# Kernel optimization log

Hardware: AMD Instinct MI355X
Metric: run time of the kernel (lower is better)

## Reference

```python
import jax, jax.numpy as jnp
import numpy as np

TEMPERATURE = 0.1
NUM_CLASSES = 100


def setup_inputs() -> dict:
    key = jax.random.key(0)
    k1, k2 = jax.random.split(key)
    embeddings = jax.random.normal(k1, (8192, 128), dtype=jnp.float32)
    labels = jax.random.randint(k2, (8192,), 0, NUM_CLASSES, dtype=jnp.int64)
    return {"embeddings": embeddings, "labels": labels}


def reference(embeddings, labels):
    # L2-normalize rows (eps matches torch.nn.functional.normalize clamp)
    norm = jnp.maximum(jnp.linalg.norm(embeddings, axis=1, keepdims=True), 1e-12)
    e = embeddings / norm
    sim = jnp.matmul(e, e.T) / TEMPERATURE  # [N, N]
    n = sim.shape[0]
    eye = jnp.eye(n, dtype=bool)
    # positives: same label, excluding self
    pos = (labels[None, :] == labels[:, None]) & ~eye
    # The per-row torch loop computes soft-target cross-entropy over all
    # non-diagonal entries: row_loss_i = -sum_{j in pos(i)} log_softmax(sim[i, j!=i])_j.
    # log_softmax is permutation-invariant, so concatenation order is irrelevant.
    neg_inf = jnp.finfo(sim.dtype).min
    masked = jnp.where(eye, neg_inf, sim)
    logz = jax.nn.logsumexp(masked, axis=1, keepdims=True)  # [N, 1]
    logp = sim - logz  # [N, N]
    row_loss = -jnp.sum(jnp.where(pos, logp, 0.0), axis=1)  # rows with no positives contribute 0
    return jnp.sum(row_loss) / n
```

## Files before the change

kernel.cpp:

```cpp
#include <hip/hip_runtime.h>


#define N 8192
#define D 128
#define NCLS 100
#define RLCAP 256
#define JSPLIT 32
#define IBLK 256
#define NJT ((N / JSPLIT) / 16)
#define K2E 14.4269504088896340736f
#define LN2 0.69314718055994530942f

typedef __bf16 bf16x8 __attribute__((ext_vector_type(8)));
typedef float f32x4 __attribute__((ext_vector_type(4)));

#define EBF_OFF  0x000000u
#define ENORM_OFF 0x200000u
#define CNT_OFF  0x600000u
#define Z_OFF    0x600200u
#define RL_OFF   0x608200u
#define S_OFF    0x621200u
#define ZERO_SZ  (512u + 32768u)

__device__ __forceinline__ unsigned short f32_to_bf16_rne(float f) {
    unsigned int u = __float_as_uint(f);
    u += 0x7fffu + ((u >> 16) & 1u);
    return (unsigned short)(u >> 16);
}


__global__ __launch_bounds__(256) void prep_kernel(
        const float* __restrict__ emb, const int* __restrict__ labels,
        unsigned char* __restrict__ ebf, int* __restrict__ cnt,
        float* __restrict__ enorm, int* __restrict__ rowlist) {
    const int wave = threadIdx.x >> 6;
    const int lane = threadIdx.x & 63;
    const int row  = blockIdx.x * 4 + wave;

    const float2 v = *(const float2*)(emb + (size_t)row * D + lane * 2);
    float ss = v.x * v.x + v.y * v.y;
    #pragma unroll
    for (int off = 32; off; off >>= 1) ss += __shfl_xor(ss, off);
    const float inv = 1.0f / fmaxf(sqrtf(ss), 1e-12f);
    const float ex = v.x * inv, ey = v.y * inv;

    const int grp = row >> 4, col = row & 15;
    const int c = lane >> 4, q = (lane >> 2) & 3, j2 = lane & 3;
    unsigned int packed = (unsigned int)f32_to_bf16_rne(ex) |
                          ((unsigned int)f32_to_bf16_rne(ey) << 16);
    *(unsigned int*)(ebf + grp * 4096 + c * 1024 + q * 256 + col * 16 + j2 * 4) = packed;

    float2* ep = (float2*)(enorm + (size_t)row * D + lane * 2);
    *ep = make_float2(ex, ey);

    if (lane == 0) {
        const int lab = labels[row];
        int slot = atomicAdd(&cnt[lab], 1);
        slot = slot < RLCAP ? slot : RLCAP - 1;
        rowlist[lab * RLCAP + slot] = row;
    }
}

__global__ __launch_bounds__(128) void classsum_kernel(
        const float* __restrict__ enorm, const int* __restrict__ cnt,
        const int* __restrict__ rowlist, float* __restrict__ S) {
    const int c = blockIdx.x;
    const int d = threadIdx.x;
    const int n = cnt[c] < RLCAP ? cnt[c] : RLCAP;
    const int* rl = rowlist + c * RLCAP;
    float acc = 0.0f;
    int idx = 0;
    for (; idx + 4 <= n; idx += 4) {
        const int r0 = rl[idx], r1 = rl[idx + 1], r2 = rl[idx + 2], r3 = rl[idx + 3];
        const float v0 = enorm[(size_t)r0 * D + d];
        const float v1 = enorm[(size_t)r1 * D + d];
        const float v2 = enorm[(size_t)r2 * D + d];
        const float v3 = enorm[(size_t)r3 * D + d];
        acc += v0 + v1 + v2 + v3;
    }
    for (; idx < n; ++idx)
        acc += enorm[(size_t)rl[idx] * D + d];
    S[c * D + d] = acc;
}

__global__ __launch_bounds__(256) void zsum_kernel(
        const unsigned char* __restrict__ ebf, float* __restrict__ z) {
    const int t    = threadIdx.x;
    const int w    = t >> 6;
    const int lane = t & 63;
    const int q    = lane >> 4;
    const int col  = lane & 15;
    const int iw   = blockIdx.x * IBLK + w * 64;
    const int jb   = blockIdx.y * (N / JSPLIT);

    bf16x8 a[4][4];
    #pragma unroll
    for (int g = 0; g < 4; ++g) {
        const unsigned char* ag = ebf + (size_t)(iw / 16 + g) * 4096 + lane * 16;
        #pragma unroll
        for (int c = 0; c < 4; ++c) a[g][c] = *(const bf16x8*)(ag + c * 1024);
    }

    float zacc[4][4] = {{0.f,0.f,0.f,0.f},{0.f,0.f,0.f,0.f},
                        {0.f,0.f,0.f,0.f},{0.f,0.f,0.f,0.f}};

    const unsigned char* bbase = ebf + (size_t)(jb / 16) * 4096 + lane * 16;

    bf16x8 bc[4];
    #pragma unroll
    for (int c = 0; c < 4; ++c) bc[c] = *(const bf16x8*)(bbase + c * 1024);

    #pragma unroll 2
    for (int jt = 0; jt < NJT; ++jt) {
        const int js = jb + jt * 16;

        const int jn = (jt + 1 < NJT) ? jt + 1 : jt;
        bf16x8 bn[4];
        {
            const unsigned char* bg = bbase + (size_t)jn * 4096;
            #pragma unroll
            for (int c = 0; c < 4; ++c) bn[c] = *(const bf16x8*)(bg + c * 1024);
        }

        #pragma unroll
        for (int g = 0; g < 4; ++g) {
            f32x4 acc = {0.f, 0.f, 0.f, 0.f};
            __builtin_amdgcn_s_setprio(1);
            #pragma unroll
            for (int c = 0; c < 4; ++c)
                acc = __builtin_amdgcn_mfma_f32_16x16x32_bf16(a[g][c], bc[c], acc, 0, 0, 0);
            __builtin_amdgcn_s_setprio(0);
            if (js == iw + g * 16) {
                #pragma unroll
                for (int r = 0; r < 4; ++r)
                    zacc[g][r] += (col == q * 4 + r) ? 0.0f
                        : __builtin_amdgcn_exp2f(fmaf(acc[r], K2E, -K2E));
            } else {
                #pragma unroll
                for (int r = 0; r < 4; ++r)
                    zacc[g][r] += __builtin_amdgcn_exp2f(fmaf(acc[r], K2E, -K2E));
            }
        }

        #pragma unroll
        for (int c = 0; c < 4; ++c) bc[c] = bn[c];
    }

    #pragma unroll
    for (int g = 0; g < 4; ++g)
        #pragma unroll
        for (int r = 0; r < 4; ++r) {
            float zv = zacc[g][r];
            zv += __shfl_xor(zv, 1);
            zv += __shfl_xor(zv, 2);
            zv += __shfl_xor(zv, 4);
            zv += __shfl_xor(zv, 8);
            if (col == 0)
                atomicAdd(&z[iw + g * 16 + q * 4 + r], zv);
        }
}

__global__ __launch_bounds__(1024) void final_kernel(
        const int* __restrict__ labels, const int* __restrict__ cnt,
        const float* __restrict__ z, const float* __restrict__ S,
        float* __restrict__ out) {
    __shared__ float part[16];
    const int tid = threadIdx.x;
    float acc = 0.0f;
    #pragma unroll
    for (int k = 0; k < N / 1024; ++k) {
        const int row = k * 1024 + tid;
        const int P = cnt[labels[row]] - 1;
        if (P > 0)
            acc += (float)P * fmaf(LN2, __builtin_amdgcn_logf(z[row]), 10.0f);
    }
    #pragma unroll
    for (int k = 0; k < (NCLS * D + 1023) / 1024; ++k) {
        const int idx = k * 1024 + tid;
        if (idx < NCLS * D) {
            const float sv = S[idx];
            acc -= 10.0f * sv * sv;
        }
    }
    #pragma unroll
    for (int off = 32; off; off >>= 1) acc += __shfl_xor(acc, off);
    if ((tid & 63) == 0) part[tid >> 6] = acc;
    __syncthreads();
    if (tid == 0) {
        float tot = 0.0f;
        #pragma unroll
        for (int w = 0; w < 16; ++w) tot += part[w];
        out[0] = (tot + 10.0f * (float)N) * (1.0f / (float)N);
    }
}

extern "C" void kernel_launch(void* const* d_in, const int* in_sizes, int n_in,
                              void* d_out, int out_size, void* d_ws, size_t ws_size,
                              hipStream_t stream) {
    const float* emb  = (const float*)d_in[0];
    const int* labels = (const int*)d_in[1];
    float* out        = (float*)d_out;
    char* ws          = (char*)d_ws;

    unsigned char* ebf = (unsigned char*)(ws + EBF_OFF);
    float* enorm       = (float*)(ws + ENORM_OFF);
    int*   cnt         = (int*)(ws + CNT_OFF);
    float* z           = (float*)(ws + Z_OFF);
    int*   rowlist     = (int*)(ws + RL_OFF);
    float* S           = (float*)(ws + S_OFF);

    hipMemsetAsync(ws + CNT_OFF, 0, ZERO_SZ, stream);

    prep_kernel<<<N / 4, 256, 0, stream>>>(emb, labels, ebf, cnt, enorm, rowlist);
    classsum_kernel<<<NCLS, 128, 0, stream>>>(enorm, cnt, rowlist, S);
    zsum_kernel<<<dim3(N / IBLK, JSPLIT), 256, 0, stream>>>(ebf, z);
    final_kernel<<<1, 1024, 0, stream>>>(labels, cnt, z, S, out);
}
```

Before: 127.1 us.

## Exploit Gram matrix symmetry to halve MFMA and exp work in zsum

The z-sum kernel now computes only the upper-triangle tile pairs of the symmetric similarity matrix, using a circulant offset scheme over 512 row tiles. Each computed tile contributes its exponentials both to its own rows and, through column sums reduced in LDS and via atomics, to the mirrored rows. This is meant to roughly halve the matrix-multiply and exp2 work. In exchange it adds column reductions, more atomics and tricky tile-distance bookkeeping, which carries some risk of load imbalance.

New measurement: 125.1 us. Within noise of the previous version (-1.6%).

```diff
diff --git a/kernel.cpp b/kernel.cpp
--- a/kernel.cpp
+++ b/kernel.cpp
@@ -4,10 +4,12 @@
 #define N 8192
 #define D 128
 #define NCLS 100
+#define NTILE 512
 #define RLCAP 256
-#define JSPLIT 32
 #define IBLK 256
-#define NJT ((N / JSPLIT) / 16)
+#define MWIN 8
+#define YGRID 32
+#define LDS_TILES 20
 #define K2E 14.4269504088896340736f
 #define LN2 0.69314718055994530942f
 
@@ -72,11 +74,8 @@
     int idx = 0;
     for (; idx + 4 <= n; idx += 4) {
         const int r0 = rl[idx], r1 = rl[idx + 1], r2 = rl[idx + 2], r3 = rl[idx + 3];
-        const float v0 = enorm[(size_t)r0 * D + d];
-        const float v1 = enorm[(size_t)r1 * D + d];
-        const float v2 = enorm[(size_t)r2 * D + d];
-        const float v3 = enorm[(size_t)r3 * D + d];
-        acc += v0 + v1 + v2 + v3;
+        acc += enorm[(size_t)r0 * D + d] + enorm[(size_t)r1 * D + d]
+             + enorm[(size_t)r2 * D + d] + enorm[(size_t)r3 * D + d];
     }
     for (; idx < n; ++idx)
         acc += enorm[(size_t)rl[idx] * D + d];
@@ -85,18 +84,24 @@
 
 __global__ __launch_bounds__(256) void zsum_kernel(
         const unsigned char* __restrict__ ebf, float* __restrict__ z) {
+    __shared__ float zcol[LDS_TILES * 16];
     const int t    = threadIdx.x;
     const int w    = t >> 6;
     const int lane = t & 63;
     const int q    = lane >> 4;
     const int col  = lane & 15;
-    const int iw   = blockIdx.x * IBLK + w * 64;
-    const int jb   = blockIdx.y * (N / JSPLIT);
+    const int bi   = blockIdx.x;
+    const int y    = blockIdx.y;
+    const int ti0  = bi * 16 + w * 4;
+    const int m_lo = y * MWIN + 1;
+    const bool lowhalf = (bi < 16);
+
+    for (int e = t; e < LDS_TILES * 16; e += 256) zcol[e] = 0.0f;
 
     bf16x8 a[4][4];
     #pragma unroll
     for (int g = 0; g < 4; ++g) {
-        const unsigned char* ag = ebf + (size_t)(iw / 16 + g) * 4096 + lane * 16;
+        const unsigned char* ag = ebf + (size_t)(ti0 + g) * 4096 + lane * 16;
         #pragma unroll
         for (int c = 0; c < 4; ++c) a[g][c] = *(const bf16x8*)(ag + c * 1024);
     }
@@ -104,41 +109,81 @@
     float zacc[4][4] = {{0.f,0.f,0.f,0.f},{0.f,0.f,0.f,0.f},
                         {0.f,0.f,0.f,0.f},{0.f,0.f,0.f,0.f}};
 
-    const unsigned char* bbase = ebf + (size_t)(jb / 16) * 4096 + lane * 16;
+    __syncthreads();
+
+    if (y == 0) {
+        #pragma unroll
+        for (int g = 0; g < 4; ++g) {
+            const unsigned char* bg = ebf + (size_t)(ti0 + g) * 4096 + lane * 16;
+            bf16x8 bd[4];
+            #pragma unroll
+            for (int c = 0; c < 4; ++c) bd[c] = *(const bf16x8*)(bg + c * 1024);
+            f32x4 acc = {0.f, 0.f, 0.f, 0.f};
+            #pragma unroll
+            for (int c = 0; c < 4; ++c)
+                acc = __builtin_amdgcn_mfma_f32_16x16x32_bf16(a[g][c], bd[c], acc, 0, 0, 0);
+            #pragma unroll
+            for (int r = 0; r < 4; ++r)
+                zacc[g][r] += (col == q * 4 + r) ? 0.0f
+                    : __builtin_amdgcn_exp2f(fmaf(acc[r], K2E, -K2E));
+        }
+    }
+
+    const int ns = MWIN + ((y == 29 || y == 30 || (y == 31 && lowhalf)) ? 1 : 0);
+    const int m_x = 228 + y;
 
     bf16x8 bc[4];
-    #pragma unroll
-    for (int c = 0; c < 4; ++c) bc[c] = *(const bf16x8*)(bbase + c * 1024);
+    {
+        const int tj = (ti0 + m_lo) & (NTILE - 1);
+        const unsigned char* bg = ebf + (size_t)tj * 4096 + lane * 16;
+        #pragma unroll
+        for (int c = 0; c < 4; ++c) bc[c] = *(const bf16x8*)(bg + c * 1024);
+    }
 
     #pragma unroll 2
-    for (int jt = 0; jt < NJT; ++jt) {
-        const int js = jb + jt * 16;
-
-        const int jn = (jt + 1 < NJT) ? jt + 1 : jt;
+    for (int s = 0; s < ns; ++s) {
+        const int m = (s < MWIN) ? (m_lo + s) : m_x;
+
+        const int sn = (s + 1 < ns) ? s + 1 : s;
+        const int mn = (sn < MWIN) ? (m_lo + sn) : m_x;
         bf16x8 bn[4];
         {
-            const unsigned char* bg = bbase + (size_t)jn * 4096;
+            const int tjn = (ti0 + mn) & (NTILE - 1);
+            const unsigned char* bg = ebf + (size_t)tjn * 4096 + lane * 16;
             #pragma unroll
             for (int c = 0; c < 4; ++c) bn[c] = *(const bf16x8*)(bg + c * 1024);
         }
 
+        float ctot = 0.0f;
         #pragma unroll
         for (int g = 0; g < 4; ++g) {
-            f32x4 acc = {0.f, 0.f, 0.f, 0.f};
-            __builtin_amdgcn_s_setprio(1);
-            #pragma unroll
-            for (int c = 0; c < 4; ++c)
-                acc = __builtin_amdgcn_mfma_f32_16x16x32_bf16(a[g][c], bc[c], acc, 0, 0, 0);
-            __builtin_amdgcn_s_setprio(0);
-            if (js == iw + g * 16) {
+            const int d = m - g;
+            const bool act = (d >= 1 && d <= 255) || (d == 256 && lowhalf);
+            if (act) {
+                f32x4 acc = {0.f, 0.f, 0.f, 0.f};
+                __builtin_amdgcn_s_setprio(1);
                 #pragma unroll
-                for (int r = 0; r < 4; ++r)
-                    zacc[g][r] += (col == q * 4 + r) ? 0.0f
-                        : __builtin_amdgcn_exp2f(fmaf(acc[r], K2E, -K2E));
+                for (int c = 0; c < 4; ++c)
+                    acc = __builtin_amdgcn_mfma_f32_16x16x32_bf16(a[g][c], bc[c], acc, 0, 0, 0);
+                __builtin_amdgcn_s_setprio(0);
+                #pragma unroll
+                for (int r = 0; r < 4; ++r) {
+                    const float p = __builtin_amdgcn_exp2f(fmaf(acc[r], K2E, -K2E));
+                    zacc[g][r] += p;
+                    ctot += p;
+                }
+            }
+        }
+
+        ctot += __shfl_xor(ctot, 16);
+        ctot += __shfl_xor(ctot, 32);
+        if (q == 0 && ctot != 0.0f) {
+            if (s < MWIN) {
+                const int rel = w * 4 + (m - m_lo);
+                atomicAdd(&zcol[rel * 16 + col], ctot);
             } else {
-                #pragma unroll
-                for (int r = 0; r < 4; ++r)
-                    zacc[g][r] += __builtin_amdgcn_exp2f(fmaf(acc[r], K2E, -K2E));
+                const int tj = (ti0 + m) & (NTILE - 1);
+                atomicAdd(&z[tj * 16 + col], ctot);
             }
         }
 
@@ -156,8 +201,17 @@
             zv += __shfl_xor(zv, 4);
             zv += __shfl_xor(zv, 8);
             if (col == 0)
-                atomicAdd(&z[iw + g * 16 + q * 4 + r], zv);
-        }
+                atomicAdd(&z[(ti0 + g) * 16 + q * 4 + r], zv);
+        }
+
+    __syncthreads();
+    for (int e = t; e < LDS_TILES * 16; e += 256) {
+        const float v = zcol[e];
+        if (v != 0.0f) {
+            const int tj = (bi * 16 + m_lo + (e >> 4)) & (NTILE - 1);
+            atomicAdd(&z[tj * 16 + (e & 15)], v);
+        }
+    }
 }
 
 __global__ __launch_bounds__(1024) void final_kernel(
@@ -213,6 +267,6 @@
 
     prep_kernel<<<N / 4, 256, 0, stream>>>(emb, labels, ebf, cnt, enorm, rowlist);
     classsum_kernel<<<NCLS, 128, 0, stream>>>(enorm, cnt, rowlist, S);
-    zsum_kernel<<<dim3(N / IBLK, JSPLIT), 256, 0, stream>>>(ebf, z);
+    zsum_kernel<<<dim3(N / IBLK, YGRID), 256, 0, stream>>>(ebf, z);
     final_kernel<<<1, 1024, 0, stream>>>(labels, cnt, z, S, out);
 }
```
